# Kernel optimization log

Hardware: AMD Instinct MI355X
Metric: run time of the kernel (lower is better)

Reference implementation:

```python
import jax, jax.numpy as jnp
import numpy as np

S_MAX = 1.5


def grid_sample_bilinear(feat, grid):
    """torch F.grid_sample, bilinear, align_corners=True, padding_mode='zeros'.
    feat: [B,C,H,W]; grid: [B,T,2] in [-1,1] (x=width coord, y=height coord).
    Returns [B,T,C]."""
    B, C, H, W = feat.shape
    ix = (grid[..., 0] + 1.0) * 0.5 * (W - 1)  # [B,T]
    iy = (grid[..., 1] + 1.0) * 0.5 * (H - 1)
    ix0 = jnp.floor(ix); iy0 = jnp.floor(iy)
    wx1 = ix - ix0; wx0 = 1.0 - wx1
    wy1 = iy - iy0; wy0 = 1.0 - wy1

    def gather(yy, xx):
        valid = (xx >= 0) & (xx <= W - 1) & (yy >= 0) & (yy <= H - 1)  # [B,T]
        xc = jnp.clip(xx, 0, W - 1).astype(jnp.int32)
        yc = jnp.clip(yy, 0, H - 1).astype(jnp.int32)
        vals = jax.vmap(lambda f, y, x: f[:, y, x])(feat, yc, xc)  # [B,C,T]
        return vals * valid[:, None, :].astype(feat.dtype)

    g00 = gather(iy0, ix0); g01 = gather(iy0, ix0 + 1)
    g10 = gather(iy0 + 1, ix0); g11 = gather(iy0 + 1, ix0 + 1)
    out = (g00 * (wy0 * wx0)[:, None, :] + g01 * (wy0 * wx1)[:, None, :]
           + g10 * (wy1 * wx0)[:, None, :] + g11 * (wy1 * wx1)[:, None, :])
    return jnp.transpose(out, (0, 2, 1))  # [B,T,C]


def _mlp(h, i, W0, b0, W1, b1, W2, b2):
    # 5-layer MLP with SiLU, params stacked over the 4 STNets on axis 0
    h = jax.nn.silu(h @ W0[i].T + b0[i])
    for j in range(3):
        h = jax.nn.silu(h @ W1[i, j].T + b1[i, j])
    return h @ W2[i].T + b2[i]


def _st_pair(z_keep, w, cond, cur_z, idx_s, idx_t, params):
    # one grid_sample shared between the s and t nets (same current_z)
    lf = grid_sample_bilinear(w, cur_z * 2.0 - 1.0)  # [B,T,C]
    B, T, _ = z_keep.shape
    cb = jnp.broadcast_to(cond[:, None, :], (B, T, cond.shape[-1]))
    comb = jnp.concatenate([z_keep, lf, cb], axis=-1)
    s = jnp.tanh(_mlp(comb, idx_s, *params)) * S_MAX
    t = _mlp(comb, idx_t, *params)
    return s, t


def setup_inputs() -> dict:
    key = jax.random.key(0)
    ks = jax.random.split(key, 9)
    B, T, C, H, W = 64, 4096, 64, 64, 64
    COND, HID = 16, 128
    in_dim = 1 + C + COND
    x = jax.random.uniform(ks[0], (B, T, 2), dtype=jnp.float32)
    w = jax.random.normal(ks[1], (B, C, H, W), dtype=jnp.float32)
    cond = jax.random.normal(ks[2], (B, COND), dtype=jnp.float32)
    # params stacked over nets: 0=s_a, 1=t_a, 2=s_b, 3=t_b
    W0 = jax.random.normal(ks[3], (4, HID, in_dim)) / np.sqrt(in_dim)
    b0 = jax.random.normal(ks[4], (4, HID)) * 0.01
    W1 = jax.random.normal(ks[5], (4, 3, HID, HID)) / np.sqrt(HID)
    b1 = jax.random.normal(ks[6], (4, 3, HID)) * 0.01
    # torch inits the last layer to zero; use small random values instead for a
    # non-degenerate correctness baseline
    W2 = jax.random.normal(ks[7], (4, 1, HID)) * 0.01
    b2 = jax.random.normal(ks[8], (4, 1)) * 0.01
    return dict(x=x, w=w, cond=cond, W0=W0, b0=b0, W1=W1, b1=b1, W2=W2, b2=b2)


def reference(x, w, cond, W0, b0, W1, b1, W2, b2):
    params = (W0, b0, W1, b1, W2, b2)
    z_a = x[:, :, 0:1]
    z_b = x[:, :, 1:2]
    s_a, t_a = _st_pair(z_b, w, cond, x, 0, 1, params)
    z_a = z_a * jnp.exp(s_a) + t_a
    _x = jnp.concatenate([z_a, z_b], axis=-1)
    s_b, t_b = _st_pair(z_a, w, cond, _x, 2, 3, params)
    z_b = z_b * jnp.exp(s_b) + t_b
    z = jnp.concatenate([z_a, z_b], axis=-1)
    log_det = s_a.sum(axis=(1, 2)) + s_b.sum(axis=(1, 2))
    return z, log_det
```

## Files before the change

kernel.cpp:

```cpp
#include <hip/hip_runtime.h>
#include <hip/hip_fp16.h>


#define NPTS (64 * 4096)
#define ZSIZE (NPTS * 2)

typedef _Float16 f16x8 __attribute__((ext_vector_type(8)));
typedef float f32x4 __attribute__((ext_vector_type(4)));

#define W0F_HALFS (4 * 3 * 8 * 1024)
#define W1F_HALFS (12 * 4 * 8 * 1024)
#define WT_BYTES_OFF ((W0F_HALFS + W1F_HALFS) * 2)
#define WT_BYTES (64ull * 64 * 64 * 64 * 4)

__global__ void prep_kernel(const float* __restrict__ W0, const float* __restrict__ W1,
                            _Float16* __restrict__ W0f, _Float16* __restrict__ W1f,
                            float* __restrict__ out_ld) {
    const int t0 = blockIdx.x * blockDim.x + threadIdx.x;
    const int stride = gridDim.x * blockDim.x;
    if (t0 < 64) out_ld[t0] = 0.f;
    for (int t = t0; t < 4 * 3 * 8 * 64 * 8; t += stride) {
        int j = t & 7, r = t >> 3;
        int l = r & 63; r >>= 6;
        int n0 = r & 7; r >>= 3;
        int kt = r % 3, idx = r / 3;
        int k = kt * 32 + (l >> 4) * 8 + j;
        int n = n0 * 16 + (l & 15);
        float v = 0.f;
        if (k <= 80) {
            int ko = (k < 80) ? (k + 1) : 0;
            v = W0[(idx * 128 + n) * 81 + ko];
        }
        _Float16 hi = (_Float16)v;
        _Float16 lo = (_Float16)(v - (float)hi);
        int base = ((idx * 3 + kt) * 8 + n0) * 1024;
        W0f[base + l * 8 + j] = hi;
        W0f[base + 512 + l * 8 + j] = lo;
    }
    for (int t = t0; t < 12 * 4 * 8 * 64 * 8; t += stride) {
        int j = t & 7, r = t >> 3;
        int l = r & 63; r >>= 6;
        int n0 = r & 7; r >>= 3;
        int kt = r & 3, m = r >> 2;
        int k = kt * 32 + (l >> 4) * 8 + j;
        int n = n0 * 16 + (l & 15);
        float v = W1[(m * 128 + n) * 128 + k];
        _Float16 hi = (_Float16)v;
        _Float16 lo = (_Float16)(v - (float)hi);
        int base = ((m * 4 + kt) * 8 + n0) * 1024;
        W1f[base + l * 8 + j] = hi;
        W1f[base + 512 + l * 8 + j] = lo;
    }
}

__global__ __launch_bounds__(256) void transpose_w(const float* __restrict__ w,
                                                   float* __restrict__ wt) {
    __shared__ float t[64][65];
    const int by = blockIdx.x;
    const int y = by & 63, b = by >> 6;
    const int c4 = threadIdx.x >> 6, xx = threadIdx.x & 63;
    const float* src = w + ((size_t)b << 18) + ((size_t)y << 6);
#pragma unroll
    for (int i = 0; i < 16; ++i) {
        const int c = i * 4 + c4;
        t[c][xx] = src[((size_t)c << 12) + xx];
    }
    __syncthreads();
    float* dst = wt + ((size_t)b << 18) + ((size_t)y << 12);
#pragma unroll
    for (int i = 0; i < 16; ++i) {
        const int xo = i * 4 + c4;
        dst[(xo << 6) + xx] = t[xx][xo];
    }
}

template <int KT, bool LO>
__device__ __forceinline__ void load_bfrag(f16x8* B, const _Float16* __restrict__ wfb,
                                           int n0, int lane) {
#pragma unroll
    for (int kt = 0; kt < KT; ++kt) {
        const _Float16* c2 = wfb + kt * 8192 + n0 * 1024 + lane * 8;
        if (LO) {
            B[2 * kt] = *(const f16x8*)c2;
            B[2 * kt + 1] = *(const f16x8*)(c2 + 512);
        } else {
            B[kt] = *(const f16x8*)c2;
        }
    }
}

template <int KT, bool LO>
__device__ __forceinline__ void mfma_n0(const f16x8* A, const f16x8* B, float bb,
                                        f32x4& acc0, f32x4& acc1) {
    acc0 = (f32x4){bb, bb, bb, bb};
    acc1 = (f32x4){bb, bb, bb, bb};
#pragma unroll
    for (int kt = 0; kt < KT; ++kt) {
        const f16x8 bh = B[LO ? 2 * kt : kt];
        acc0 = __builtin_amdgcn_mfma_f32_16x16x32_f16(A[kt], bh, acc0, 0, 0, 0);
        acc1 = __builtin_amdgcn_mfma_f32_16x16x32_f16(A[KT + kt], bh, acc1, 0, 0, 0);
        if (LO) {
            const f16x8 bl = B[2 * kt + 1];
            acc0 = __builtin_amdgcn_mfma_f32_16x16x32_f16(A[kt], bl, acc0, 0, 0, 0);
            acc1 = __builtin_amdgcn_mfma_f32_16x16x32_f16(A[KT + kt], bl, acc1, 0, 0, 0);
        }
    }
}

__device__ __forceinline__ float silu(float v) {
    return v * __builtin_amdgcn_rcpf(1.f + __expf(-v));
}

template <int KT, bool LO>
__device__ __forceinline__ void run_layer(const f16x8* A, const _Float16* __restrict__ wfb,
                                          const float* __restrict__ bias,
                                          _Float16 (*hrow)[136], int lane, int fr, int fg) {
#pragma unroll
    for (int n0 = 0; n0 < 8; ++n0) {
        f16x8 B[LO ? 2 * KT : KT];
        load_bfrag<KT, LO>(B, wfb, n0, lane);
        f32x4 acc0, acc1;
        mfma_n0<KT, LO>(A, B, bias[n0 * 16 + fr], acc0, acc1);
#pragma unroll
        for (int t2 = 0; t2 < 2; ++t2) {
            const f32x4 a = t2 ? acc1 : acc0;
#pragma unroll
            for (int rg = 0; rg < 4; ++rg)
                hrow[t2 * 16 + fg * 4 + rg][n0 * 16 + fr] = (_Float16)silu(a[rg]);
        }
    }
}

template <int KT, bool LO>
__device__ __forceinline__ void run_layer_final(const f16x8* A, const _Float16* __restrict__ wfb,
                                                const float* __restrict__ bias,
                                                const float* w2v, float* dotp, int lane, int fr) {
#pragma unroll
    for (int n0 = 0; n0 < 8; ++n0) {
        f16x8 B[LO ? 2 * KT : KT];
        load_bfrag<KT, LO>(B, wfb, n0, lane);
        f32x4 acc0, acc1;
        mfma_n0<KT, LO>(A, B, bias[n0 * 16 + fr], acc0, acc1);
#pragma unroll
        for (int t2 = 0; t2 < 2; ++t2) {
            const f32x4 a = t2 ? acc1 : acc0;
#pragma unroll
            for (int rg = 0; rg < 4; ++rg)
                dotp[t2 * 4 + rg] = fmaf(silu(a[rg]), w2v[n0], dotp[t2 * 4 + rg]);
        }
    }
}

template <bool LO>
__device__ __forceinline__ void mlp_chain(int idx, const f16x8* cfr,
                                          const _Float16* __restrict__ W0f,
                                          const float* __restrict__ b0,
                                          const _Float16* __restrict__ W1f,
                                          const float* __restrict__ b1,
                                          const float* __restrict__ W2,
                                          const float* __restrict__ b2,
                                          _Float16 (*hrow)[136], float* hyrow, int lane, int fr,
                                          int fg) {
    run_layer<3, LO>(cfr, W0f + idx * 3 * 8192, b0 + idx * 128, hrow, lane, fr, fg);
#pragma unroll
    for (int l = 0; l < 2; ++l) {
        f16x8 afr[8];
#pragma unroll
        for (int t2 = 0; t2 < 2; ++t2)
#pragma unroll
            for (int kt = 0; kt < 4; ++kt)
                afr[t2 * 4 + kt] = *(const f16x8*)&hrow[t2 * 16 + fr][kt * 32 + fg * 8];
        run_layer<4, LO>(afr, W1f + (idx * 3 + l) * 4 * 8192, b1 + (idx * 3 + l) * 128, hrow,
                         lane, fr, fg);
    }
    {
        f16x8 afr[8];
#pragma unroll
        for (int t2 = 0; t2 < 2; ++t2)
#pragma unroll
            for (int kt = 0; kt < 4; ++kt)
                afr[t2 * 4 + kt] = *(const f16x8*)&hrow[t2 * 16 + fr][kt * 32 + fg * 8];
        float w2v[8];
#pragma unroll
        for (int n0 = 0; n0 < 8; ++n0) w2v[n0] = W2[idx * 128 + n0 * 16 + fr];
        float dotp[8];
#pragma unroll
        for (int i = 0; i < 8; ++i) dotp[i] = 0.f;
        run_layer_final<4, LO>(afr, W1f + (idx * 3 + 2) * 4 * 8192, b1 + (idx * 3 + 2) * 128,
                               w2v, dotp, lane, fr);
#pragma unroll
        for (int off = 1; off <= 8; off <<= 1)
#pragma unroll
            for (int i = 0; i < 8; ++i) dotp[i] += __shfl_xor(dotp[i], off);
        if (fr == 0) {
            const float b2v = b2[idx];
#pragma unroll
            for (int t2 = 0; t2 < 2; ++t2)
#pragma unroll
                for (int rg = 0; rg < 4; ++rg)
                    hyrow[t2 * 16 + fg * 4 + rg] = dotp[t2 * 4 + rg] + b2v;
        }
    }
}

template <bool FIRST>
__device__ __forceinline__ void tap_acc(float* lf, const float* __restrict__ tp, float f) {
#pragma unroll
    for (int r = 0; r < 8; ++r) {
        const f32x4 v = *(const f32x4*)(tp + 4 * r);
#pragma unroll
        for (int j = 0; j < 4; ++j)
            lf[4 * r + j] = FIRST ? f * v[j] : fmaf(f, v[j], lf[4 * r + j]);
    }
    __builtin_amdgcn_sched_barrier(0);
}

template <bool TR>
__global__ __launch_bounds__(128, 2) void fused_kernel(
    const float* __restrict__ x, const float* __restrict__ w, const float* __restrict__ wt,
    const float* __restrict__ cond, const _Float16* __restrict__ W0f,
    const float* __restrict__ b0, const _Float16* __restrict__ W1f,
    const float* __restrict__ b1, const float* __restrict__ W2, const float* __restrict__ b2,
    float* __restrict__ out) {
    __shared__ __align__(16) _Float16 hlds[2][32][136];
    __shared__ float hy[2][2][32];

    const int o = blockIdx.x;
    const int wg = (o & 7) * 512 + (o >> 3);
    const int tid = threadIdx.x;
    const int wv = tid >> 6, lane = tid & 63;
    const int pl = lane & 31;
    const int hh = lane >> 5;
    const int fr = lane & 15, fg = lane >> 4;
    const int pbase = wg * 64 + wv * 32;
    const int b = wg >> 6;

    const float2 xv = *(const float2*)&x[2 * (pbase + pl)];
    const float xa = xv.x, xb = xv.y;
    float za = 0.f, zb = 0.f;

    __half2 cpk[8];
    {
        const float* cb = cond + b * 16;
#pragma unroll
        for (int j = 0; j < 8; ++j) cpk[j] = __floats2half2_rn(cb[2 * j], cb[2 * j + 1]);
    }

    float s_acc = 0.f;

    for (int stage = 0; stage < 2; ++stage) {
        const float cx = stage ? za : xa;
        const float cy = xb;
        const float gx = cx * 2.f - 1.f, gy = cy * 2.f - 1.f;
        const float ixf = (gx + 1.f) * 0.5f * 63.f;
        const float iyf = (gy + 1.f) * 0.5f * 63.f;
        const float ix0f = floorf(ixf), iy0f = floorf(iyf);
        const float ix1f = ix0f + 1.f, iy1f = iy0f + 1.f;
        const float wx1 = ixf - ix0f, wx0 = 1.f - wx1;
        const float wy1 = iyf - iy0f, wy0 = 1.f - wy1;
        const bool vx0 = (ix0f >= 0.f) && (ix0f <= 63.f);
        const bool vx1 = (ix1f >= 0.f) && (ix1f <= 63.f);
        const bool vy0 = (iy0f >= 0.f) && (iy0f <= 63.f);
        const bool vy1 = (iy1f >= 0.f) && (iy1f <= 63.f);
        const float f00 = (vy0 && vx0) ? wy0 * wx0 : 0.f;
        const float f01 = (vy0 && vx1) ? wy0 * wx1 : 0.f;
        const float f10 = (vy1 && vx0) ? wy1 * wx0 : 0.f;
        const float f11 = (vy1 && vx1) ? wy1 * wx1 : 0.f;
        const int xi0 = (int)fminf(fmaxf(ix0f, 0.f), 63.f);
        const int xi1 = (int)fminf(fmaxf(ix1f, 0.f), 63.f);
        const int yi0 = (int)fminf(fmaxf(iy0f, 0.f), 63.f);
        const int yi1 = (int)fminf(fmaxf(iy1f, 0.f), 63.f);
        const int o00 = yi0 * 64 + xi0, o01 = yi0 * 64 + xi1;
        const int o10 = yi1 * 64 + xi0, o11 = yi1 * 64 + xi1;

        if (TR) {
            const float* wtb = wt + ((size_t)b << 18) + hh * 32;
            float lf[32];
            tap_acc<true>(lf, wtb + ((size_t)o00 << 6), f00);
            tap_acc<false>(lf, wtb + ((size_t)o01 << 6), f01);
            tap_acc<false>(lf, wtb + ((size_t)o10 << 6), f10);
            tap_acc<false>(lf, wtb + ((size_t)o11 << 6), f11);
#pragma unroll
            for (int j = 0; j < 16; ++j)
                *(__half2*)&hlds[wv][pl][hh * 32 + 2 * j] =
                    __floats2half2_rn(lf[2 * j], lf[2 * j + 1]);
        } else {
            const float* wq = w + ((size_t)b << 18) + ((size_t)hh << 17);
#pragma unroll 4
            for (int jj = 0; jj < 16; ++jj) {
                const float* wcA = wq + ((2 * jj) << 12);
                const float* wcB = wcA + 4096;
                const float lfA =
                    f00 * wcA[o00] + f01 * wcA[o01] + f10 * wcA[o10] + f11 * wcA[o11];
                const float lfB =
                    f00 * wcB[o00] + f01 * wcB[o01] + f10 * wcB[o10] + f11 * wcB[o11];
                *(__half2*)&hlds[wv][pl][hh * 32 + 2 * jj] = __floats2half2_rn(lfA, lfB);
            }
        }
        if (hh == 0) {
            const float zk = stage ? za : xb;
#pragma unroll
            for (int j2 = 0; j2 < 8; ++j2) *(__half2*)&hlds[wv][pl][64 + 2 * j2] = cpk[j2];
            *(__half2*)&hlds[wv][pl][80] = __floats2half2_rn(zk, 0.f);
#pragma unroll
            for (int j2 = 41; j2 < 48; ++j2)
                *(__half2*)&hlds[wv][pl][2 * j2] = __floats2half2_rn(0.f, 0.f);
        }

        f16x8 cfr[6];
#pragma unroll
        for (int t2 = 0; t2 < 2; ++t2)
#pragma unroll
            for (int kt = 0; kt < 3; ++kt)
                cfr[t2 * 3 + kt] = *(const f16x8*)&hlds[wv][t2 * 16 + fr][kt * 32 + fg * 8];

        mlp_chain<true>(stage * 2 + 0, cfr, W0f, b0, W1f, b1, W2, b2, hlds[wv], &hy[wv][0][0],
                        lane, fr, fg);
        mlp_chain<false>(stage * 2 + 1, cfr, W0f, b0, W1f, b1, W2, b2, hlds[wv], &hy[wv][1][0],
                         lane, fr, fg);

        const float ys = hy[wv][0][pl];
        const float yt = hy[wv][1][pl];
        const float s = 1.5f * (1.f - 2.f * __builtin_amdgcn_rcpf(__expf(2.f * ys) + 1.f));
        if (stage == 0)
            za = fmaf(xa, __expf(s), yt);
        else
            zb = fmaf(xb, __expf(s), yt);
        if (hh == 0) s_acc += s;
    }

    if (hh == 0) *(float2*)&out[2 * (pbase + pl)] = make_float2(za, zb);

    float r = s_acc;
#pragma unroll
    for (int off = 1; off <= 32; off <<= 1) r += __shfl_xor(r, off);
    if (lane == 0) atomicAdd(out + ZSIZE + b, r);
}

extern "C" void kernel_launch(void* const* d_in, const int* in_sizes, int n_in,
                              void* d_out, int out_size, void* d_ws, size_t ws_size,
                              hipStream_t stream) {
    const float* x = (const float*)d_in[0];
    const float* w = (const float*)d_in[1];
    const float* cond = (const float*)d_in[2];
    const float* W0 = (const float*)d_in[3];
    const float* b0 = (const float*)d_in[4];
    const float* W1 = (const float*)d_in[5];
    const float* b1 = (const float*)d_in[6];
    const float* W2 = (const float*)d_in[7];
    const float* b2 = (const float*)d_in[8];
    float* out = (float*)d_out;

    _Float16* W0f = (_Float16*)d_ws;
    _Float16* W1f = W0f + W0F_HALFS;
    float* wt = (float*)((char*)d_ws + WT_BYTES_OFF);
    const bool big = ws_size >= (size_t)WT_BYTES_OFF + WT_BYTES;

    prep_kernel<<<256, 256, 0, stream>>>(W0, W1, W0f, W1f, out + ZSIZE);
    if (big) {
        transpose_w<<<4096, 256, 0, stream>>>(w, wt);
        fused_kernel<true><<<4096, 128, 0, stream>>>(x, w, wt, cond, W0f, b0, W1f, b1, W2, b2,
                                                     out);
    } else {
        fused_kernel<false><<<4096, 128, 0, stream>>>(x, w, wt, cond, W0f, b0, W1f, b1, W2, b2,
                                                      out);
    }
}
```

Measured before the change: 411.2 us.

## Keep MLP activations in registers by computing transposed MFMA layers

Swaps the MFMA operand roles so weights act as the A operand and activations as B. Each layer's output accumulators can then be SiLU-packed straight into the next layer's B fragments in registers instead of round-tripping through LDS. The W1 fragment layout in prep is permuted to match the new k ordering, and the final dot product reduces with two cross-lane shuffles. It also drops the non-transposed fallback path, so the transpose workspace is now always assumed, and the larger accumulator arrays raise register pressure.

```diff
diff --git a/kernel.cpp b/kernel.cpp
--- a/kernel.cpp
+++ b/kernel.cpp
@@ -6,6 +6,8 @@
 #define ZSIZE (NPTS * 2)
 
 typedef _Float16 f16x8 __attribute__((ext_vector_type(8)));
+typedef _Float16 f16x2 __attribute__((ext_vector_type(2)));
+typedef __fp16 fp16x2 __attribute__((ext_vector_type(2)));
 typedef float f32x4 __attribute__((ext_vector_type(4)));
 
 #define W0F_HALFS (4 * 3 * 8 * 1024)
@@ -42,7 +44,7 @@
         int l = r & 63; r >>= 6;
         int n0 = r & 7; r >>= 3;
         int kt = r & 3, m = r >> 2;
-        int k = kt * 32 + (l >> 4) * 8 + j;
+        int k = kt * 32 + ((j >> 2) << 4) + ((l >> 4) << 2) + (j & 3);
         int n = n0 * 16 + (l & 15);
         float v = W1[(m * 128 + n) * 128 + k];
         _Float16 hi = (_Float16)v;
@@ -74,133 +76,108 @@
     }
 }
 
-template <int KT, bool LO>
-__device__ __forceinline__ void load_bfrag(f16x8* B, const _Float16* __restrict__ wfb,
-                                           int n0, int lane) {
-#pragma unroll
-    for (int kt = 0; kt < KT; ++kt) {
-        const _Float16* c2 = wfb + kt * 8192 + n0 * 1024 + lane * 8;
-        if (LO) {
-            B[2 * kt] = *(const f16x8*)c2;
-            B[2 * kt + 1] = *(const f16x8*)(c2 + 512);
-        } else {
-            B[kt] = *(const f16x8*)c2;
-        }
-    }
-}
-
-template <int KT, bool LO>
-__device__ __forceinline__ void mfma_n0(const f16x8* A, const f16x8* B, float bb,
-                                        f32x4& acc0, f32x4& acc1) {
-    acc0 = (f32x4){bb, bb, bb, bb};
-    acc1 = (f32x4){bb, bb, bb, bb};
-#pragma unroll
-    for (int kt = 0; kt < KT; ++kt) {
-        const f16x8 bh = B[LO ? 2 * kt : kt];
-        acc0 = __builtin_amdgcn_mfma_f32_16x16x32_f16(A[kt], bh, acc0, 0, 0, 0);
-        acc1 = __builtin_amdgcn_mfma_f32_16x16x32_f16(A[KT + kt], bh, acc1, 0, 0, 0);
-        if (LO) {
-            const f16x8 bl = B[2 * kt + 1];
-            acc0 = __builtin_amdgcn_mfma_f32_16x16x32_f16(A[kt], bl, acc0, 0, 0, 0);
-            acc1 = __builtin_amdgcn_mfma_f32_16x16x32_f16(A[KT + kt], bl, acc1, 0, 0, 0);
-        }
-    }
-}
-
 __device__ __forceinline__ float silu(float v) {
     return v * __builtin_amdgcn_rcpf(1.f + __expf(-v));
 }
 
-template <int KT, bool LO>
-__device__ __forceinline__ void run_layer(const f16x8* A, const _Float16* __restrict__ wfb,
-                                          const float* __restrict__ bias,
-                                          _Float16 (*hrow)[136], int lane, int fr, int fg) {
+__device__ __forceinline__ f16x2 cvt2(float a, float b) {
+    union {
+        fp16x2 n;
+        f16x2 t;
+    } u;
+    u.n = __builtin_amdgcn_cvt_pkrtz(a, b);
+    return u.t;
+}
+
+__device__ __forceinline__ f16x8 pack_silu(f32x4 aA, f32x4 aB) {
+    union {
+        f16x2 h2[4];
+        f16x8 v;
+    } u;
+    u.h2[0] = cvt2(silu(aA[0]), silu(aA[1]));
+    u.h2[1] = cvt2(silu(aA[2]), silu(aA[3]));
+    u.h2[2] = cvt2(silu(aB[0]), silu(aB[1]));
+    u.h2[3] = cvt2(silu(aB[2]), silu(aB[3]));
+    return u.v;
+}
+
+template <bool LO, int KT>
+__device__ __forceinline__ void layer_mfma(const _Float16* __restrict__ wfb,
+                                           const float* __restrict__ bias,
+                                           const f16x8 (*Bin)[4], f32x4 (*acc)[8], int lane,
+                                           int fg) {
 #pragma unroll
     for (int n0 = 0; n0 < 8; ++n0) {
-        f16x8 B[LO ? 2 * KT : KT];
-        load_bfrag<KT, LO>(B, wfb, n0, lane);
-        f32x4 acc0, acc1;
-        mfma_n0<KT, LO>(A, B, bias[n0 * 16 + fr], acc0, acc1);
-#pragma unroll
-        for (int t2 = 0; t2 < 2; ++t2) {
-            const f32x4 a = t2 ? acc1 : acc0;
-#pragma unroll
-            for (int rg = 0; rg < 4; ++rg)
-                hrow[t2 * 16 + fg * 4 + rg][n0 * 16 + fr] = (_Float16)silu(a[rg]);
-        }
-    }
-}
-
-template <int KT, bool LO>
-__device__ __forceinline__ void run_layer_final(const f16x8* A, const _Float16* __restrict__ wfb,
-                                                const float* __restrict__ bias,
-                                                const float* w2v, float* dotp, int lane, int fr) {
+        f16x8 Ah[KT];
+        f16x8 Al[KT];
+#pragma unroll
+        for (int kt = 0; kt < KT; ++kt) {
+            const _Float16* c2 = wfb + (kt * 8 + n0) * 1024 + lane * 8;
+            Ah[kt] = *(const f16x8*)c2;
+            if (LO) Al[kt] = *(const f16x8*)(c2 + 512);
+        }
+        const f32x4 b4 = *(const f32x4*)(bias + n0 * 16 + 4 * fg);
+        f32x4 a0 = b4, a1 = b4;
+#pragma unroll
+        for (int kt = 0; kt < KT; ++kt) {
+            a0 = __builtin_amdgcn_mfma_f32_16x16x32_f16(Ah[kt], Bin[0][kt], a0, 0, 0, 0);
+            a1 = __builtin_amdgcn_mfma_f32_16x16x32_f16(Ah[kt], Bin[1][kt], a1, 0, 0, 0);
+            if (LO) {
+                a0 = __builtin_amdgcn_mfma_f32_16x16x32_f16(Al[kt], Bin[0][kt], a0, 0, 0, 0);
+                a1 = __builtin_amdgcn_mfma_f32_16x16x32_f16(Al[kt], Bin[1][kt], a1, 0, 0, 0);
+            }
+        }
+        acc[0][n0] = a0;
+        acc[1][n0] = a1;
+    }
+}
+
+template <bool LO>
+__device__ __forceinline__ float2 mlp_chain(int idx, const _Float16* __restrict__ comb,
+                                            const _Float16* __restrict__ W0f,
+                                            const float* __restrict__ b0,
+                                            const _Float16* __restrict__ W1f,
+                                            const float* __restrict__ b1,
+                                            const float* __restrict__ W2,
+                                            const float* __restrict__ b2, int lane, int fr,
+                                            int fg) {
+    f32x4 acc[2][8];
+    {
+        f16x8 cB[2][4];
+#pragma unroll
+        for (int pt = 0; pt < 2; ++pt)
+#pragma unroll
+            for (int kt = 0; kt < 3; ++kt)
+                cB[pt][kt] = *(const f16x8*)(comb + (pt * 16 + fr) * 104 + kt * 32 + fg * 8);
+        layer_mfma<LO, 3>(W0f + idx * 3 * 8192, b0 + idx * 128, cB, acc, lane, fg);
+    }
+    f16x8 hB[2][4];
+#pragma unroll
+    for (int l = 0; l < 3; ++l) {
+#pragma unroll
+        for (int pt = 0; pt < 2; ++pt)
+#pragma unroll
+            for (int kt = 0; kt < 4; ++kt)
+                hB[pt][kt] = pack_silu(acc[pt][2 * kt], acc[pt][2 * kt + 1]);
+        layer_mfma<LO, 4>(W1f + (idx * 3 + l) * 32768, b1 + (idx * 3 + l) * 128, hB, acc, lane,
+                          fg);
+    }
+    float d0 = 0.f, d1 = 0.f;
 #pragma unroll
     for (int n0 = 0; n0 < 8; ++n0) {
-        f16x8 B[LO ? 2 * KT : KT];
-        load_bfrag<KT, LO>(B, wfb, n0, lane);
-        f32x4 acc0, acc1;
-        mfma_n0<KT, LO>(A, B, bias[n0 * 16 + fr], acc0, acc1);
-#pragma unroll
-        for (int t2 = 0; t2 < 2; ++t2) {
-            const f32x4 a = t2 ? acc1 : acc0;
-#pragma unroll
-            for (int rg = 0; rg < 4; ++rg)
-                dotp[t2 * 4 + rg] = fmaf(silu(a[rg]), w2v[n0], dotp[t2 * 4 + rg]);
-        }
-    }
-}
-
-template <bool LO>
-__device__ __forceinline__ void mlp_chain(int idx, const f16x8* cfr,
-                                          const _Float16* __restrict__ W0f,
-                                          const float* __restrict__ b0,
-                                          const _Float16* __restrict__ W1f,
-                                          const float* __restrict__ b1,
-                                          const float* __restrict__ W2,
-                                          const float* __restrict__ b2,
-                                          _Float16 (*hrow)[136], float* hyrow, int lane, int fr,
-                                          int fg) {
-    run_layer<3, LO>(cfr, W0f + idx * 3 * 8192, b0 + idx * 128, hrow, lane, fr, fg);
-#pragma unroll
-    for (int l = 0; l < 2; ++l) {
-        f16x8 afr[8];
-#pragma unroll
-        for (int t2 = 0; t2 < 2; ++t2)
-#pragma unroll
-            for (int kt = 0; kt < 4; ++kt)
-                afr[t2 * 4 + kt] = *(const f16x8*)&hrow[t2 * 16 + fr][kt * 32 + fg * 8];
-        run_layer<4, LO>(afr, W1f + (idx * 3 + l) * 4 * 8192, b1 + (idx * 3 + l) * 128, hrow,
-                         lane, fr, fg);
-    }
-    {
-        f16x8 afr[8];
-#pragma unroll
-        for (int t2 = 0; t2 < 2; ++t2)
-#pragma unroll
-            for (int kt = 0; kt < 4; ++kt)
-                afr[t2 * 4 + kt] = *(const f16x8*)&hrow[t2 * 16 + fr][kt * 32 + fg * 8];
-        float w2v[8];
-#pragma unroll
-        for (int n0 = 0; n0 < 8; ++n0) w2v[n0] = W2[idx * 128 + n0 * 16 + fr];
-        float dotp[8];
-#pragma unroll
-        for (int i = 0; i < 8; ++i) dotp[i] = 0.f;
-        run_layer_final<4, LO>(afr, W1f + (idx * 3 + 2) * 4 * 8192, b1 + (idx * 3 + 2) * 128,
-                               w2v, dotp, lane, fr);
-#pragma unroll
-        for (int off = 1; off <= 8; off <<= 1)
-#pragma unroll
-            for (int i = 0; i < 8; ++i) dotp[i] += __shfl_xor(dotp[i], off);
-        if (fr == 0) {
-            const float b2v = b2[idx];
-#pragma unroll
-            for (int t2 = 0; t2 < 2; ++t2)
-#pragma unroll
-                for (int rg = 0; rg < 4; ++rg)
-                    hyrow[t2 * 16 + fg * 4 + rg] = dotp[t2 * 4 + rg] + b2v;
-        }
-    }
+        const f32x4 w2v = *(const f32x4*)(W2 + idx * 128 + n0 * 16 + 4 * fg);
+#pragma unroll
+        for (int rg = 0; rg < 4; ++rg) {
+            d0 = fmaf(silu(acc[0][n0][rg]), w2v[rg], d0);
+            d1 = fmaf(silu(acc[1][n0][rg]), w2v[rg], d1);
+        }
+    }
+    d0 += __shfl_xor(d0, 16);
+    d0 += __shfl_xor(d0, 32);
+    d1 += __shfl_xor(d1, 16);
+    d1 += __shfl_xor(d1, 32);
+    const float b2v = b2[idx];
+    return make_float2(d0 + b2v, d1 + b2v);
 }
 
 template <bool FIRST>
@@ -215,15 +192,12 @@
     __builtin_amdgcn_sched_barrier(0);
 }
 
-template <bool TR>
 __global__ __launch_bounds__(128, 2) void fused_kernel(
-    const float* __restrict__ x, const float* __restrict__ w, const float* __restrict__ wt,
-    const float* __restrict__ cond, const _Float16* __restrict__ W0f,
-    const float* __restrict__ b0, const _Float16* __restrict__ W1f,
-    const float* __restrict__ b1, const float* __restrict__ W2, const float* __restrict__ b2,
-    float* __restrict__ out) {
-    __shared__ __align__(16) _Float16 hlds[2][32][136];
-    __shared__ float hy[2][2][32];
+    const float* __restrict__ x, const float* __restrict__ wt, const float* __restrict__ cond,
+    const _Float16* __restrict__ W0f, const float* __restrict__ b0,
+    const _Float16* __restrict__ W1f, const float* __restrict__ b1,
+    const float* __restrict__ W2, const float* __restrict__ b2, float* __restrict__ out) {
+    __shared__ __align__(16) _Float16 clds[2][32][104];
 
     const int o = blockIdx.x;
     const int wg = (o & 7) * 512 + (o >> 3);
@@ -273,7 +247,7 @@
         const int o00 = yi0 * 64 + xi0, o01 = yi0 * 64 + xi1;
         const int o10 = yi1 * 64 + xi0, o11 = yi1 * 64 + xi1;
 
-        if (TR) {
+        {
             const float* wtb = wt + ((size_t)b << 18) + hh * 32;
             float lf[32];
             tap_acc<true>(lf, wtb + ((size_t)o00 << 6), f00);
@@ -282,45 +256,27 @@
             tap_acc<false>(lf, wtb + ((size_t)o11 << 6), f11);
 #pragma unroll
             for (int j = 0; j < 16; ++j)
-                *(__half2*)&hlds[wv][pl][hh * 32 + 2 * j] =
+                *(__half2*)&clds[wv][pl][hh * 32 + 2 * j] =
                     __floats2half2_rn(lf[2 * j], lf[2 * j + 1]);
-        } else {
-            const float* wq = w + ((size_t)b << 18) + ((size_t)hh << 17);
-#pragma unroll 4
-            for (int jj = 0; jj < 16; ++jj) {
-                const float* wcA = wq + ((2 * jj) << 12);
-                const float* wcB = wcA + 4096;
-                const float lfA =
-                    f00 * wcA[o00] + f01 * wcA[o01] + f10 * wcA[o10] + f11 * wcA[o11];
-                const float lfB =
-                    f00 * wcB[o00] + f01 * wcB[o01] + f10 * wcB[o10] + f11 * wcB[o11];
-                *(__half2*)&hlds[wv][pl][hh * 32 + 2 * jj] = __floats2half2_rn(lfA, lfB);
-            }
         }
         if (hh == 0) {
             const float zk = stage ? za : xb;
 #pragma unroll
-            for (int j2 = 0; j2 < 8; ++j2) *(__half2*)&hlds[wv][pl][64 + 2 * j2] = cpk[j2];
-            *(__half2*)&hlds[wv][pl][80] = __floats2half2_rn(zk, 0.f);
+            for (int j2 = 0; j2 < 8; ++j2) *(__half2*)&clds[wv][pl][64 + 2 * j2] = cpk[j2];
+            *(__half2*)&clds[wv][pl][80] = __floats2half2_rn(zk, 0.f);
 #pragma unroll
             for (int j2 = 41; j2 < 48; ++j2)
-                *(__half2*)&hlds[wv][pl][2 * j2] = __floats2half2_rn(0.f, 0.f);
-        }
-
-        f16x8 cfr[6];
-#pragma unroll
-        for (int t2 = 0; t2 < 2; ++t2)
-#pragma unroll
-            for (int kt = 0; kt < 3; ++kt)
-                cfr[t2 * 3 + kt] = *(const f16x8*)&hlds[wv][t2 * 16 + fr][kt * 32 + fg * 8];
-
-        mlp_chain<true>(stage * 2 + 0, cfr, W0f, b0, W1f, b1, W2, b2, hlds[wv], &hy[wv][0][0],
-                        lane, fr, fg);
-        mlp_chain<false>(stage * 2 + 1, cfr, W0f, b0, W1f, b1, W2, b2, hlds[wv], &hy[wv][1][0],
-                         lane, fr, fg);
-
-        const float ys = hy[wv][0][pl];
-        const float yt = hy[wv][1][pl];
+                *(__half2*)&clds[wv][pl][2 * j2] = __floats2half2_rn(0.f, 0.f);
+        }
+
+        const _Float16* comb = &clds[wv][0][0];
+        const float2 ys2 = mlp_chain<true>(stage * 2 + 0, comb, W0f, b0, W1f, b1, W2, b2, lane,
+                                           fr, fg);
+        const float2 yt2 = mlp_chain<false>(stage * 2 + 1, comb, W0f, b0, W1f, b1, W2, b2, lane,
+                                            fr, fg);
+
+        const float ys = (pl < 16) ? ys2.x : ys2.y;
+        const float yt = (pl < 16) ? yt2.x : yt2.y;
         const float s = 1.5f * (1.f - 2.f * __builtin_amdgcn_rcpf(__expf(2.f * ys) + 1.f));
         if (stage == 0)
             za = fmaf(xa, __expf(s), yt);
@@ -354,15 +310,8 @@
     _Float16* W0f = (_Float16*)d_ws;
     _Float16* W1f = W0f + W0F_HALFS;
     float* wt = (float*)((char*)d_ws + WT_BYTES_OFF);
-    const bool big = ws_size >= (size_t)WT_BYTES_OFF + WT_BYTES;
 
     prep_kernel<<<256, 256, 0, stream>>>(W0, W1, W0f, W1f, out + ZSIZE);
-    if (big) {
-        transpose_w<<<4096, 256, 0, stream>>>(w, wt);
-        fused_kernel<true><<<4096, 128, 0, stream>>>(x, w, wt, cond, W0f, b0, W1f, b1, W2, b2,
-                                                     out);
-    } else {
-        fused_kernel<false><<<4096, 128, 0, stream>>>(x, w, wt, cond, W0f, b0, W1f, b1, W2, b2,
-                                                      out);
-    }
-}
+    transpose_w<<<4096, 256, 0, stream>>>(w, wt);
+    fused_kernel<<<4096, 128, 0, stream>>>(x, wt, cond, W0f, b0, W1f, b1, W2, b2, out);
+}
```

After: 479.5 us. +16.6%, slower.
